# Kernel optimization log

Hardware: AMD Instinct MI355X
Metric: run time of the kernel (lower is better)

## Reference

```python
import jax, jax.numpy as jnp
import numpy as np
from jax import lax

# module hyperparams (from init_kwargs)
IN_C, OUT_C, K, STRIDE, PAD, DIL = 256, 512, 3, 1, 1, 1
IN_SIZE = IN_C * K * K            # 2304
SIZE = 1 << int(np.ceil(np.log2(IN_SIZE)))  # 4096, in_size_extended
NSTACK = int(np.ceil(OUT_C / SIZE))          # 1
BATCH, H, W = 16, 32, 32


def fwht(x):
    """Unnormalized fast Walsh-Hadamard transform along last axis (n = power of 2).
    Matches torch.mm(hadamard(n), x.T).T / cyfht. O(n log n) butterfly."""
    n = x.shape[-1]
    orig_shape = x.shape
    x = x.reshape(-1, n)
    h = 1
    while h < n:
        x = x.reshape(-1, n // (2 * h), 2, h)
        a, b = x[:, :, 0, :], x[:, :, 1, :]
        x = jnp.stack([a + b, a - b], axis=2).reshape(-1, n)
        h *= 2
    return x.reshape(orig_shape)


def setup_inputs() -> dict:
    key = jax.random.key(0)
    k1, k2, k3, k4, k5, k6 = jax.random.split(key, 6)
    inp = jax.random.normal(k1, (BATCH, IN_C, H, W), dtype=jnp.float32)
    # B, G, S ~ N(0, 0.1) as in __init__
    B = 0.1 * jax.random.normal(k2, (NSTACK, SIZE), dtype=jnp.float32)
    G = 0.1 * jax.random.normal(k3, (NSTACK, SIZE), dtype=jnp.float32)
    S = 0.1 * jax.random.normal(k4, (NSTACK, SIZE), dtype=jnp.float32)
    bound = 1.0 / np.sqrt(IN_SIZE)
    bias = jax.random.uniform(k5, (OUT_C,), minval=-bound, maxval=bound, dtype=jnp.float32)
    P = jax.random.permutation(k6, NSTACK * SIZE)  # int32 permutation buffer
    return {"input": inp, "B": B, "G": G, "S": S, "bias": bias, "P": P}


def _pre_process(x):
    b, c, h, w = x.shape
    h_out = (h + 2 * PAD - DIL * (K - 1) - 1) // STRIDE + 1
    w_out = (h + 2 * PAD - DIL * (K - 1) - 1) // STRIDE + 1  # original uses h for w_out too
    # patches: (b, c*K*K, h_out, w_out), feature dim ordered (c, kh, kw) like F.unfold
    patches = lax.conv_general_dilated_patches(
        x, (K, K), (STRIDE, STRIDE), [(PAD, PAD), (PAD, PAD)],
        rhs_dilation=(DIL, DIL), dimension_numbers=("NCHW", "OIHW", "NCHW"))
    # view(b, c, K*K, L).permute(0,3,2,1).reshape(b*L, K*K*c)  -> kk-major, c-minor features
    L = h_out * w_out
    out = patches.reshape(b, c, K * K, L).transpose(0, 3, 2, 1).reshape(b * L, K * K * c)
    out = jnp.pad(out, ((0, 0), (0, SIZE - IN_SIZE)))
    return out, h_out, w_out


def reference(input, B, G, S, bias, P):
    b = input.shape[0]
    x, h_out, w_out = _pre_process(input)          # (b*L, SIZE)
    # diag B (nstack=1), FWHT, permutation, diag G, FWHT, diag S
    x = B.reshape(-1)[None, :] * x
    x = fwht(x)
    x = x[:, P]
    x = G.reshape(-1)[None, :] * x
    x = fwht(x)
    x = S.reshape(-1)[None, :] * x
    out = x[:, :OUT_C] + bias                      # (b*L, OUT_C)
    return out.reshape(b, h_out * w_out, OUT_C).transpose(0, 2, 1).reshape(b, OUT_C, h_out, w_out)
```

## Files before the change

kernel.cpp:

```cpp
#include <hip/hip_runtime.h>
#include <hip/hip_bf16.h>
#include <stdint.h>


typedef _Float16 h2 __attribute__((ext_vector_type(2)));

__device__ __forceinline__ uint16_t f2h16(float f) {
    union { _Float16 h; uint16_t u; } c; c.h = (_Float16)f; return c.u;
}
__device__ __forceinline__ float h16f(uint16_t u) {
    union { _Float16 h; uint16_t u; } c; c.u = u; return (float)c.h;
}
__device__ __forceinline__ int swz(int j) {
    return j ^ ((j >> 5) & 7) ^ (((j >> 8) & 1) * 24) ^ (((j >> 9) & 1) * 8);
}
__device__ __forceinline__ uint32_t h2u(h2 v) {
    union { h2 h; uint32_t u; } c; c.h = v; return c.u;
}
__device__ __forceinline__ h2 u2h(uint32_t x) {
    union { h2 h; uint32_t u; } c; c.u = x; return c.h;
}
__device__ __forceinline__ h2 pkh(float a, float b) {
    h2 r; r.x = (_Float16)a; r.y = (_Float16)b; return r;
}
__device__ __forceinline__ void h16h(h2* x) {
    #pragma unroll
    for (int h = 1; h < 16; h <<= 1) {
        #pragma unroll
        for (int g = 0; g < 16; g += 2 * h) {
            #pragma unroll
            for (int u = g; u < g + h; ++u) {
                h2 a = x[u], b = x[u + h];
                x[u]     = a + b;
                x[u + h] = a - b;
            }
        }
    }
}
__device__ __forceinline__ void trunc16(const h2* x, h2& s, h2& d) {
    h2 sp[8], sm[8];
    #pragma unroll
    for (int i = 0; i < 8; ++i) {
        sp[i] = x[2 * i] + x[2 * i + 1];
        sm[i] = x[2 * i] - x[2 * i + 1];
    }
    #pragma unroll
    for (int h = 4; h >= 1; h >>= 1) {
        #pragma unroll
        for (int i = 0; i < h; ++i) { sp[i] = sp[i] + sp[i + h]; sm[i] = sm[i] + sm[i + h]; }
    }
    s = sp[0]; d = sm[0];
}
__device__ __forceinline__ _Float16 slotk(const uint2& u, int k) {
    const h2 a = u2h(u.x), c = u2h(u.y);
    return (k == 0) ? a.x : (k == 1) ? c.x : (k == 2) ? a.y : c.y;
}

__global__ __launch_bounds__(256, 2)
void fastfood_kernel(const float* __restrict__ in,
                     const float* __restrict__ Bm,
                     const float* __restrict__ Gm,
                     const float* __restrict__ Sm,
                     const float* __restrict__ bias,
                     const int* __restrict__ P,
                     float* __restrict__ out)
{
    __shared__ __align__(16) uint16_t s_in[3 * 8 * 256 * 4];
    __shared__ __align__(16) uint2    bufA[4096];

    const int t  = threadIdx.x;
    const int t1 = t >> 4, t0 = t & 15;
    const int b  = blockIdx.x >> 5;
    const int oh = blockIdx.x & 31;

    #pragma unroll
    for (int i = 0; i < 24; ++i) {
        const int idx   = t + i * 256;
        const int part  = idx & 7;
        const int ch    = (idx >> 3) & 255;
        const int ihrel = idx >> 11;
        const int ih    = oh - 1 + ihrel;
        float4 ld = make_float4(0.f, 0.f, 0.f, 0.f);
        if ((unsigned)ih < 32u) {
            ld = *reinterpret_cast<const float4*>(
                in + ((((size_t)b * 256 + ch) * 32 + ih) * 32 + part * 4));
        }
        const int q    = part >> 1;
        const int slot = (q == 0) ? 0 : (q == 1) ? 2 : (q == 2) ? 1 : 3;
        const int g0   = 4 * (part & 1);
        const int base = (ihrel * 8 + g0) * 1024 + ch * 4 + slot;
        s_in[base       ] = f2h16(ld.x);
        s_in[base + 1024] = f2h16(ld.y);
        s_in[base + 2048] = f2h16(ld.z);
        s_in[base + 3072] = f2h16(ld.w);
    }

    float Bf[9];
    #pragma unroll
    for (int r = 0; r < 9; ++r) Bf[r] = Bm[r * 256 + t];
    h2 Bh[9];
    #pragma unroll
    for (int r = 0; r < 9; ++r) Bh[r] = pkh(Bf[r], Bf[r]);

    h2 Gh[16]; int PAv[16];
    #pragma unroll
    for (int q = 0; q < 4; ++q) {
        const int4   pv = *reinterpret_cast<const int4*>(P + 16 * t + 4 * q);
        const float4 gv = *reinterpret_cast<const float4*>(Gm + 16 * t + 4 * q);
        PAv[4 * q + 0] = swz(pv.x); PAv[4 * q + 1] = swz(pv.y);
        PAv[4 * q + 2] = swz(pv.z); PAv[4 * q + 3] = swz(pv.w);
        Gh[4 * q + 0] = pkh(gv.x, gv.x); Gh[4 * q + 1] = pkh(gv.y, gv.y);
        Gh[4 * q + 2] = pkh(gv.z, gv.z); Gh[4 * q + 3] = pkh(gv.w, gv.w);
    }
    __syncthreads();

    const uint2* s2 = reinterpret_cast<const uint2*>(s_in);
    uint2 tap[3][8];
    #pragma unroll
    for (int kh = 0; kh < 3; ++kh)
        #pragma unroll
        for (int g = 0; g < 8; ++g)
            tap[kh][g] = s2[(kh * 8 + g) * 256 + t];
    uint2* bufB = reinterpret_cast<uint2*>(s_in);

    uint2 os[8], od[8];

    #pragma unroll
    for (int p = 0; p < 8; ++p) {
        h2 x0[16], x1[16];
        #pragma unroll
        for (int r = 0; r < 9; ++r) {
            const int kh = r / 3, kw = r % 3;
            const int iw = p - 1 + kw;
            const uint2 u = tap[kh][iw & 7];
            h2 a = u2h(u.x), c = u2h(u.y);
            h2 ta = a, tc = c;
            if (iw < 0) {
                ta.x = (_Float16)0.f; ta.y = c.x;
                tc = a;
            } else if (iw > 7) {
                ta = c;
                tc.x = a.y; tc.y = (_Float16)0.f;
            }
            x0[r] = Bh[r] * ta;
            x1[r] = Bh[r] * tc;
        }
        #pragma unroll
        for (int r = 9; r < 16; ++r) {
            x0[r] = pkh(0.f, 0.f);
            x1[r] = pkh(0.f, 0.f);
        }

        h16h(x0); h16h(x1);
        #pragma unroll
        for (int r = 0; r < 16; ++r)
            bufA[swz(256 * r + t)] = make_uint2(h2u(x0[r]), h2u(x1[r]));
        __syncthreads();
        #pragma unroll
        for (int r = 0; r < 16; ++r) {
            const uint2 u = bufA[swz(256 * t1 + 16 * r + t0)];
            x0[r] = u2h(u.x); x1[r] = u2h(u.y);
        }
        h16h(x0); h16h(x1);
        #pragma unroll
        for (int r = 0; r < 16; ++r)
            bufA[swz(256 * t1 + 16 * r + t0)] = make_uint2(h2u(x0[r]), h2u(x1[r]));
        #pragma unroll
        for (int r = 0; r < 16; ++r) {
            const uint2 u = bufA[swz(256 * t1 + 16 * t0 + r)];
            x0[r] = u2h(u.x); x1[r] = u2h(u.y);
        }
        h16h(x0); h16h(x1);
        #pragma unroll
        for (int r = 0; r < 16; ++r)
            bufA[swz(256 * t1 + 16 * t0 + r)] = make_uint2(h2u(x0[r]), h2u(x1[r]));
        __syncthreads();

        #pragma unroll
        for (int r = 0; r < 16; ++r) {
            const uint2 u = bufA[PAv[r]];
            x0[r] = Gh[r] * u2h(u.x);
            x1[r] = Gh[r] * u2h(u.y);
        }

        h16h(x0); h16h(x1);
        #pragma unroll
        for (int r = 0; r < 16; ++r)
            bufB[swz(256 * t1 + 16 * t0 + r)] = make_uint2(h2u(x0[r]), h2u(x1[r]));
        #pragma unroll
        for (int r = 0; r < 16; ++r) {
            const uint2 u = bufB[swz(256 * t1 + 16 * r + t0)];
            x0[r] = u2h(u.x); x1[r] = u2h(u.y);
        }
        h16h(x0); h16h(x1);
        #pragma unroll
        for (int r = 0; r < 16; ++r)
            bufB[swz(256 * t1 + 16 * r + t0)] = make_uint2(h2u(x0[r]), h2u(x1[r]));
        __syncthreads();
        #pragma unroll
        for (int r = 0; r < 16; ++r) {
            const uint2 u = bufB[swz(256 * r + t)];
            x0[r] = u2h(u.x); x1[r] = u2h(u.y);
        }
        h2 s0, d0, s1, d1;
        trunc16(x0, s0, d0);
        trunc16(x1, s1, d1);
        os[p] = make_uint2(h2u(s0), h2u(s1));
        od[p] = make_uint2(h2u(d0), h2u(d1));
    }

    uint2 U[8], V[8];
    #pragma unroll
    for (int i = 0; i < 8; ++i) {
        const int k = i >> 1, p0 = (i & 1) * 4;
        h2 lo, hi;
        lo.x = slotk(os[p0], k);     lo.y = slotk(os[p0 + 1], k);
        hi.x = slotk(os[p0 + 2], k); hi.y = slotk(os[p0 + 3], k);
        U[i] = make_uint2(h2u(lo), h2u(hi));
        lo.x = slotk(od[p0], k);     lo.y = slotk(od[p0 + 1], k);
        hi.x = slotk(od[p0 + 2], k); hi.y = slotk(od[p0 + 3], k);
        V[i] = make_uint2(h2u(lo), h2u(hi));
    }

    __syncthreads();
    {
        const int sw = (t >> 1) & 7;
        #pragma unroll
        for (int i = 0; i < 8; ++i) {
            bufA[(size_t)t * 8 + (i ^ sw)]         = U[i];
            bufA[(size_t)(256 + t) * 8 + (i ^ sw)] = V[i];
        }
    }
    __syncthreads();
    #pragma unroll
    for (int it = 0; it < 16; ++it) {
        const int oc = it * 32 + (t >> 3);
        const int c  = t & 7;
        const uint2 u = bufA[(size_t)oc * 8 + (c ^ ((oc >> 1) & 7))];
        const h2 lo = u2h(u.x), hi = u2h(u.y);
        const float S = Sm[oc], C = bias[oc];
        const float4 v = make_float4(S * (float)lo.x + C, S * (float)lo.y + C,
                                     S * (float)hi.x + C, S * (float)hi.y + C);
        *reinterpret_cast<float4*>(
            out + ((size_t)b * 512 + oc) * 1024 + (size_t)oh * 32 + 4 * c) = v;
    }
}

extern "C" void kernel_launch(void* const* d_in, const int* in_sizes, int n_in,
                              void* d_out, int out_size, void* d_ws, size_t ws_size,
                              hipStream_t stream) {
    const float* in   = (const float*)d_in[0];
    const float* Bm   = (const float*)d_in[1];
    const float* Gm   = (const float*)d_in[2];
    const float* Sm   = (const float*)d_in[3];
    const float* bias = (const float*)d_in[4];
    const int*   P    = (const int*)d_in[5];
    float* out = (float*)d_out;
    (void)d_ws; (void)ws_size;

    dim3 grid(16 * 32), block(256);
    fastfood_kernel<<<grid, block, 0, stream>>>(in, Bm, Gm, Sm, bias, P, out);
}
```

Before: 125.0 us.

## Split each output row across two blocks and shrink shared memory for occupancy

Doubles the grid so each block handles half of the 8 position groups in an output row, with a block-index mapping that places paired halves near each other. The input-staging buffer is merged into one 32KB shared buffer, loaded in two phases (two kernel rows, then the third), which cuts LDS per block and allows 4 blocks per CU. The cost is that both blocks of a pair load the full 3-row input tile, so global reads are duplicated, and extra barriers are added.

```diff
diff --git a/kernel.cpp b/kernel.cpp
--- a/kernel.cpp
+++ b/kernel.cpp
@@ -7,9 +7,6 @@
 
 __device__ __forceinline__ uint16_t f2h16(float f) {
     union { _Float16 h; uint16_t u; } c; c.h = (_Float16)f; return c.u;
-}
-__device__ __forceinline__ float h16f(uint16_t u) {
-    union { _Float16 h; uint16_t u; } c; c.u = u; return (float)c.h;
 }
 __device__ __forceinline__ int swz(int j) {
     return j ^ ((j >> 5) & 7) ^ (((j >> 8) & 1) * 24) ^ (((j >> 9) & 1) * 8);
@@ -56,7 +53,7 @@
     return (k == 0) ? a.x : (k == 1) ? c.x : (k == 2) ? a.y : c.y;
 }
 
-__global__ __launch_bounds__(256, 2)
+__global__ __launch_bounds__(256, 4)
 void fastfood_kernel(const float* __restrict__ in,
                      const float* __restrict__ Bm,
                      const float* __restrict__ Gm,
@@ -65,35 +62,15 @@
                      const int* __restrict__ P,
                      float* __restrict__ out)
 {
-    __shared__ __align__(16) uint16_t s_in[3 * 8 * 256 * 4];
-    __shared__ __align__(16) uint2    bufA[4096];
+    __shared__ __align__(16) uint2 bufX[4096];
+    uint16_t* s16 = reinterpret_cast<uint16_t*>(bufX);
 
     const int t  = threadIdx.x;
     const int t1 = t >> 4, t0 = t & 15;
-    const int b  = blockIdx.x >> 5;
-    const int oh = blockIdx.x & 31;
-
-    #pragma unroll
-    for (int i = 0; i < 24; ++i) {
-        const int idx   = t + i * 256;
-        const int part  = idx & 7;
-        const int ch    = (idx >> 3) & 255;
-        const int ihrel = idx >> 11;
-        const int ih    = oh - 1 + ihrel;
-        float4 ld = make_float4(0.f, 0.f, 0.f, 0.f);
-        if ((unsigned)ih < 32u) {
-            ld = *reinterpret_cast<const float4*>(
-                in + ((((size_t)b * 256 + ch) * 32 + ih) * 32 + part * 4));
-        }
-        const int q    = part >> 1;
-        const int slot = (q == 0) ? 0 : (q == 1) ? 2 : (q == 2) ? 1 : 3;
-        const int g0   = 4 * (part & 1);
-        const int base = (ihrel * 8 + g0) * 1024 + ch * 4 + slot;
-        s_in[base       ] = f2h16(ld.x);
-        s_in[base + 1024] = f2h16(ld.y);
-        s_in[base + 2048] = f2h16(ld.z);
-        s_in[base + 3072] = f2h16(ld.w);
-    }
+    const int idx = blockIdx.x;
+    const int h   = (idx >> 3) & 1;
+    const int rid = ((idx >> 4) << 3) | (idx & 7);
+    const int b   = rid >> 5, oh = rid & 31;
 
     float Bf[9];
     #pragma unroll
@@ -101,7 +78,6 @@
     h2 Bh[9];
     #pragma unroll
     for (int r = 0; r < 9; ++r) Bh[r] = pkh(Bf[r], Bf[r]);
-
     h2 Gh[16]; int PAv[16];
     #pragma unroll
     for (int q = 0; q < 4; ++q) {
@@ -112,21 +88,68 @@
         Gh[4 * q + 0] = pkh(gv.x, gv.x); Gh[4 * q + 1] = pkh(gv.y, gv.y);
         Gh[4 * q + 2] = pkh(gv.z, gv.z); Gh[4 * q + 3] = pkh(gv.w, gv.w);
     }
-    __syncthreads();
-
-    const uint2* s2 = reinterpret_cast<const uint2*>(s_in);
+
     uint2 tap[3][8];
     #pragma unroll
-    for (int kh = 0; kh < 3; ++kh)
+    for (int i = 0; i < 16; ++i) {
+        const int idx2  = t + i * 256;
+        const int part  = idx2 & 7;
+        const int ch    = (idx2 >> 3) & 255;
+        const int ihrel = idx2 >> 11;
+        const int ih    = oh - 1 + ihrel;
+        float4 ld = make_float4(0.f, 0.f, 0.f, 0.f);
+        if ((unsigned)ih < 32u) {
+            ld = *reinterpret_cast<const float4*>(
+                in + ((((size_t)b * 256 + ch) * 32 + ih) * 32 + part * 4));
+        }
+        const int qd   = part >> 1;
+        const int slot = (qd == 0) ? 0 : (qd == 1) ? 2 : (qd == 2) ? 1 : 3;
+        const int g0   = 4 * (part & 1);
+        const int base = ((ihrel * 8 + g0) << 10) + ch * 4 + slot;
+        s16[base       ] = f2h16(ld.x);
+        s16[base + 1024] = f2h16(ld.y);
+        s16[base + 2048] = f2h16(ld.z);
+        s16[base + 3072] = f2h16(ld.w);
+    }
+    __syncthreads();
+    #pragma unroll
+    for (int kh = 0; kh < 2; ++kh)
         #pragma unroll
         for (int g = 0; g < 8; ++g)
-            tap[kh][g] = s2[(kh * 8 + g) * 256 + t];
-    uint2* bufB = reinterpret_cast<uint2*>(s_in);
-
-    uint2 os[8], od[8];
-
-    #pragma unroll
-    for (int p = 0; p < 8; ++p) {
+            tap[kh][g] = bufX[(kh * 8 + g) * 256 + t];
+    __syncthreads();
+    #pragma unroll
+    for (int i = 16; i < 24; ++i) {
+        const int idx2  = t + i * 256;
+        const int part  = idx2 & 7;
+        const int ch    = (idx2 >> 3) & 255;
+        const int ih    = oh + 1;
+        float4 ld = make_float4(0.f, 0.f, 0.f, 0.f);
+        if ((unsigned)ih < 32u) {
+            ld = *reinterpret_cast<const float4*>(
+                in + ((((size_t)b * 256 + ch) * 32 + ih) * 32 + part * 4));
+        }
+        const int qd   = part >> 1;
+        const int slot = (qd == 0) ? 0 : (qd == 1) ? 2 : (qd == 2) ? 1 : 3;
+        const int g0   = 4 * (part & 1);
+        const int base = ((g0) << 10) + ch * 4 + slot;
+        s16[base       ] = f2h16(ld.x);
+        s16[base + 1024] = f2h16(ld.y);
+        s16[base + 2048] = f2h16(ld.z);
+        s16[base + 3072] = f2h16(ld.w);
+    }
+    __syncthreads();
+    #pragma unroll
+    for (int g = 0; g < 8; ++g)
+        tap[2][g] = bufX[g * 256 + t];
+    __syncthreads();
+
+    uint2 os[4], od[4];
+
+    #pragma unroll
+    for (int qq = 0; qq < 8; ++qq) {
+        if ((qq >> 2) != h) continue;
+        const int p = qq, q = qq & 3;
         h2 x0[16], x1[16];
         #pragma unroll
         for (int r = 0; r < 9; ++r) {
@@ -154,95 +177,96 @@
         h16h(x0); h16h(x1);
         #pragma unroll
         for (int r = 0; r < 16; ++r)
-            bufA[swz(256 * r + t)] = make_uint2(h2u(x0[r]), h2u(x1[r]));
-        __syncthreads();
-        #pragma unroll
-        for (int r = 0; r < 16; ++r) {
-            const uint2 u = bufA[swz(256 * t1 + 16 * r + t0)];
-            x0[r] = u2h(u.x); x1[r] = u2h(u.y);
-        }
-        h16h(x0); h16h(x1);
-        #pragma unroll
-        for (int r = 0; r < 16; ++r)
-            bufA[swz(256 * t1 + 16 * r + t0)] = make_uint2(h2u(x0[r]), h2u(x1[r]));
-        #pragma unroll
-        for (int r = 0; r < 16; ++r) {
-            const uint2 u = bufA[swz(256 * t1 + 16 * t0 + r)];
-            x0[r] = u2h(u.x); x1[r] = u2h(u.y);
-        }
-        h16h(x0); h16h(x1);
-        #pragma unroll
-        for (int r = 0; r < 16; ++r)
-            bufA[swz(256 * t1 + 16 * t0 + r)] = make_uint2(h2u(x0[r]), h2u(x1[r]));
-        __syncthreads();
-
-        #pragma unroll
-        for (int r = 0; r < 16; ++r) {
-            const uint2 u = bufA[PAv[r]];
+            bufX[swz(256 * r + t)] = make_uint2(h2u(x0[r]), h2u(x1[r]));
+        __syncthreads();
+        #pragma unroll
+        for (int r = 0; r < 16; ++r) {
+            const uint2 u = bufX[swz(256 * t1 + 16 * r + t0)];
+            x0[r] = u2h(u.x); x1[r] = u2h(u.y);
+        }
+        h16h(x0); h16h(x1);
+        #pragma unroll
+        for (int r = 0; r < 16; ++r)
+            bufX[swz(256 * t1 + 16 * r + t0)] = make_uint2(h2u(x0[r]), h2u(x1[r]));
+        #pragma unroll
+        for (int r = 0; r < 16; ++r) {
+            const uint2 u = bufX[swz(256 * t1 + 16 * t0 + r)];
+            x0[r] = u2h(u.x); x1[r] = u2h(u.y);
+        }
+        h16h(x0); h16h(x1);
+        #pragma unroll
+        for (int r = 0; r < 16; ++r)
+            bufX[swz(256 * t1 + 16 * t0 + r)] = make_uint2(h2u(x0[r]), h2u(x1[r]));
+        __syncthreads();
+
+        #pragma unroll
+        for (int r = 0; r < 16; ++r) {
+            const uint2 u = bufX[PAv[r]];
             x0[r] = Gh[r] * u2h(u.x);
             x1[r] = Gh[r] * u2h(u.y);
         }
 
         h16h(x0); h16h(x1);
-        #pragma unroll
-        for (int r = 0; r < 16; ++r)
-            bufB[swz(256 * t1 + 16 * t0 + r)] = make_uint2(h2u(x0[r]), h2u(x1[r]));
-        #pragma unroll
-        for (int r = 0; r < 16; ++r) {
-            const uint2 u = bufB[swz(256 * t1 + 16 * r + t0)];
-            x0[r] = u2h(u.x); x1[r] = u2h(u.y);
-        }
-        h16h(x0); h16h(x1);
-        #pragma unroll
-        for (int r = 0; r < 16; ++r)
-            bufB[swz(256 * t1 + 16 * r + t0)] = make_uint2(h2u(x0[r]), h2u(x1[r]));
-        __syncthreads();
-        #pragma unroll
-        for (int r = 0; r < 16; ++r) {
-            const uint2 u = bufB[swz(256 * r + t)];
+        __syncthreads();
+        #pragma unroll
+        for (int r = 0; r < 16; ++r)
+            bufX[swz(256 * t1 + 16 * t0 + r)] = make_uint2(h2u(x0[r]), h2u(x1[r]));
+        #pragma unroll
+        for (int r = 0; r < 16; ++r) {
+            const uint2 u = bufX[swz(256 * t1 + 16 * r + t0)];
+            x0[r] = u2h(u.x); x1[r] = u2h(u.y);
+        }
+        h16h(x0); h16h(x1);
+        #pragma unroll
+        for (int r = 0; r < 16; ++r)
+            bufX[swz(256 * t1 + 16 * r + t0)] = make_uint2(h2u(x0[r]), h2u(x1[r]));
+        __syncthreads();
+        #pragma unroll
+        for (int r = 0; r < 16; ++r) {
+            const uint2 u = bufX[swz(256 * r + t)];
             x0[r] = u2h(u.x); x1[r] = u2h(u.y);
         }
         h2 s0, d0, s1, d1;
         trunc16(x0, s0, d0);
         trunc16(x1, s1, d1);
-        os[p] = make_uint2(h2u(s0), h2u(s1));
-        od[p] = make_uint2(h2u(d0), h2u(d1));
-    }
-
-    uint2 U[8], V[8];
-    #pragma unroll
-    for (int i = 0; i < 8; ++i) {
-        const int k = i >> 1, p0 = (i & 1) * 4;
+        os[q] = make_uint2(h2u(s0), h2u(s1));
+        od[q] = make_uint2(h2u(d0), h2u(d1));
+    }
+
+    uint2 U[4], V[4];
+    #pragma unroll
+    for (int ii = 0; ii < 4; ++ii) {
         h2 lo, hi;
-        lo.x = slotk(os[p0], k);     lo.y = slotk(os[p0 + 1], k);
-        hi.x = slotk(os[p0 + 2], k); hi.y = slotk(os[p0 + 3], k);
-        U[i] = make_uint2(h2u(lo), h2u(hi));
-        lo.x = slotk(od[p0], k);     lo.y = slotk(od[p0 + 1], k);
-        hi.x = slotk(od[p0 + 2], k); hi.y = slotk(od[p0 + 3], k);
-        V[i] = make_uint2(h2u(lo), h2u(hi));
+        lo.x = slotk(os[0], ii); lo.y = slotk(os[1], ii);
+        hi.x = slotk(os[2], ii); hi.y = slotk(os[3], ii);
+        U[ii] = make_uint2(h2u(lo), h2u(hi));
+        lo.x = slotk(od[0], ii); lo.y = slotk(od[1], ii);
+        hi.x = slotk(od[2], ii); hi.y = slotk(od[3], ii);
+        V[ii] = make_uint2(h2u(lo), h2u(hi));
     }
 
     __syncthreads();
     {
-        const int sw = (t >> 1) & 7;
-        #pragma unroll
-        for (int i = 0; i < 8; ++i) {
-            bufA[(size_t)t * 8 + (i ^ sw)]         = U[i];
-            bufA[(size_t)(256 + t) * 8 + (i ^ sw)] = V[i];
-        }
-    }
-    __syncthreads();
-    #pragma unroll
-    for (int it = 0; it < 16; ++it) {
-        const int oc = it * 32 + (t >> 3);
-        const int c  = t & 7;
-        const uint2 u = bufA[(size_t)oc * 8 + (c ^ ((oc >> 1) & 7))];
+        const int sw = (t >> 2) & 3;
+        #pragma unroll
+        for (int ii = 0; ii < 4; ++ii) {
+            bufX[t * 4 + (ii ^ sw)]           = U[ii];
+            bufX[(256 + t) * 4 + (ii ^ sw)]   = V[ii];
+        }
+    }
+    __syncthreads();
+    #pragma unroll
+    for (int it = 0; it < 8; ++it) {
+        const int oc = it * 64 + (t >> 2);
+        const int ii = t & 3;
+        const uint2 u = bufX[oc * 4 + (ii ^ ((oc >> 2) & 3))];
         const h2 lo = u2h(u.x), hi = u2h(u.y);
         const float S = Sm[oc], C = bias[oc];
         const float4 v = make_float4(S * (float)lo.x + C, S * (float)lo.y + C,
                                      S * (float)hi.x + C, S * (float)hi.y + C);
         *reinterpret_cast<float4*>(
-            out + ((size_t)b * 512 + oc) * 1024 + (size_t)oh * 32 + 4 * c) = v;
+            out + ((size_t)b * 512 + oc) * 1024 + (size_t)oh * 32
+                + 4 * (2 * ii + h)) = v;
     }
 }
 
@@ -258,6 +282,6 @@
     float* out = (float*)d_out;
     (void)d_ws; (void)ws_size;
 
-    dim3 grid(16 * 32), block(256);
+    dim3 grid(1024), block(256);
     fastfood_kernel<<<grid, block, 0, stream>>>(in, Bm, Gm, Sm, bias, P, out);
 }
```

Measured after the change: 180.7 us. 1.45x slower.
